# Optimization experiments

Hardware: AMD Instinct MI355X
Metric: run time of the kernel (lower is better)

Reference implementation:

```python
import jax, jax.numpy as jnp
import numpy as np
from jax.scipy.special import logsumexp

# Model config: alphabet='ACGTZY', collapse='ACGTCA' -> 4 canonical bases, 2 mods
NBASE = 4
NTRANS = 2 * NBASE * (NBASE + 1)          # 40 flip-flop transition states
CAN_NMODS = np.array([1, 1, 0, 0])        # mods per canonical base (A:Y, C:Z)
SIZE = NTRANS + 1 + int(CAN_NMODS.sum())  # 43 linear outputs
LARGE_LOG_VAL = np.float32(50000.0)
T, N, INSIZE = 2000, 128, 256


def _can_indices():
    """Per-canonical-base index groups into the mod block of the linear output."""
    idx, cur = [], 0
    for nm in CAN_NMODS:
        idx.append(np.concatenate([[0], np.arange(cur + 1, cur + 1 + nm)]))
        cur += nm
    return idx

CAN_INDICES = _can_indices()


def setup_inputs() -> dict:
    key = jax.random.key(0)
    k1, k2, k3 = jax.random.split(key, 3)
    x = jax.random.normal(k1, (T, N, INSIZE), dtype=jnp.float32)
    W = jax.random.normal(k2, (SIZE, INSIZE), dtype=jnp.float32) / np.float32(INSIZE ** 0.5)
    b = jax.random.normal(k3, (SIZE,), dtype=jnp.float32) * 0.1
    return {"x": x, "W": W, "b": b}


def global_norm_flipflop(scores):
    """Log-partition of the flip-flop CRF via a sequential log-space scan.

    scores: (T, N, 2*nbase*(nbase+1)).
    """
    Tn, Nn, _ = scores.shape
    # initial state: flip states uniform, flop states ~ -inf
    fwd0 = jnp.concatenate(
        [jnp.zeros((Nn, NBASE), scores.dtype),
         jnp.full((Nn, NBASE), -LARGE_LOG_VAL, scores.dtype)], axis=1)
    logZ0 = logsumexp(fwd0, axis=1, keepdims=True)
    fwd0 = fwd0 - logZ0

    def step(carry, scores_t):
        fwd, logZ = carry
        # (N, nbase+1, 2*nbase): dest-state x source-state transition scores
        curr = fwd[:, None, :] + scores_t.reshape(Nn, NBASE + 1, 2 * NBASE)
        base1 = logsumexp(curr[:, :NBASE], axis=2)                    # to-flip states
        base2 = jnp.logaddexp(curr[:, NBASE, :NBASE],
                              curr[:, NBASE, NBASE:])                 # to-flop (stay)
        new = jnp.concatenate([base1, base2], axis=1)                 # (N, 2*nbase)
        fac = logsumexp(new, axis=1, keepdims=True)
        return (new - fac, logZ + fac), None

    (_, logZ), _ = jax.lax.scan(step, (fwd0, logZ0), scores)
    return scores - logZ / np.float32(Tn)


def reference(x, W, b):
    # Linear projection: (T, N, insize) -> (T, N, size)
    y = jnp.einsum('tnf,cf->tnc', x, W) + b
    # Globally-normalized flip-flop transition scores
    trans = global_norm_flipflop(y[:, :, :NTRANS])
    # Per-canonical-base categorical (can + its mods) log-softmax scores
    mods = [jax.nn.log_softmax(y[:, :, NTRANS + idx], axis=2) for idx in CAN_INDICES]
    return jnp.concatenate([trans] + mods, axis=2)
```

## Files before the change

kernel.cpp:

```cpp
#include <hip/hip_runtime.h>

#define T_DIM 2000
#define N_DIM 128
#define IN_DIM 256
#define OUT_C 46
#define NROWS (T_DIM * N_DIM)
#define NCHUNK 250
#define CLEN 8
#define NSUPER 25
#define SLEN 10

typedef short bf16x8 __attribute__((ext_vector_type(8)));
typedef float f32x4 __attribute__((ext_vector_type(4)));

union F8U { bf16x8 v; uint32_t u[4]; };

__device__ __forceinline__ uint32_t cvtpk(float lo, float hi) {
  uint32_t r;
  asm("v_cvt_pk_bf16_f32 %0, %1, %2" : "=v"(r) : "v"(lo), "v"(hi));
  return r;
}

__device__ __forceinline__ float bf2f(unsigned short u) {
  uint32_t w = (uint32_t)u << 16;
  return __builtin_bit_cast(float, w);
}

#define LDSK 264

__global__ __launch_bounds__(256, 4) void k1_gemm(const float* __restrict__ x,
                                                  const float* __restrict__ W,
                                                  const float* __restrict__ b,
                                                  unsigned short* __restrict__ wsYT,
                                                  float* __restrict__ wsMod) {
  __shared__ unsigned short Wl[43 * LDSK];
  const int tid  = threadIdx.x;
  const int lane = tid & 63;
  const int wv   = tid >> 6;
  const int ln   = lane & 15;
  const int lh   = lane >> 4;

  {
    uint32_t* Wd = reinterpret_cast<uint32_t*>(Wl);
#pragma unroll
    for (int it = 0; it < 22; ++it) {
      int e = tid + it * 256;
      if (e < 43 * 128) {
        int n = e >> 7, kp = e & 127;
        float2 w = *reinterpret_cast<const float2*>(W + (size_t)n * IN_DIM + 2 * kp);
        Wd[n * (LDSK / 2) + kp] = cvtpk(w.x, w.y);
      }
    }
  }
  float bias[3];
#pragma unroll
  for (int nt = 0; nt < 3; ++nt) {
    int n = nt * 16 + ln;
    bias[nt] = b[n > 42 ? 42 : n];
  }
  __syncthreads();

  const int rowbase = blockIdx.x * 256 + wv * 64;
  const float* xbase = x + (size_t)(rowbase + ln) * IN_DIM + lh * 8;

  float4 bufA[8], bufB[8];
  f32x4 zero = {0.f, 0.f, 0.f, 0.f};
  f32x4 acc[3] = {zero, zero, zero};

#define LOADH(BUF, T, HF) do {                                               \
    const float* _p = xbase + (size_t)(T) * (16 * IN_DIM) + (HF) * 128;      \
    _Pragma("unroll")                                                        \
    for (int _s = 0; _s < 4; ++_s) {                                         \
      BUF[_s]     = *reinterpret_cast<const float4*>(_p + _s * 32);          \
      BUF[_s + 4] = *reinterpret_cast<const float4*>(_p + _s * 32 + 4);      \
    }                                                                        \
  } while (0)

#define COMPH(BUF, HF) do {                                                  \
    _Pragma("unroll")                                                        \
    for (int _s2 = 0; _s2 < 4; ++_s2) {                                      \
      F8U _af;                                                               \
      _af.u[0] = cvtpk(BUF[_s2].x, BUF[_s2].y);                              \
      _af.u[1] = cvtpk(BUF[_s2].z, BUF[_s2].w);                              \
      _af.u[2] = cvtpk(BUF[_s2 + 4].x, BUF[_s2 + 4].y);                      \
      _af.u[3] = cvtpk(BUF[_s2 + 4].z, BUF[_s2 + 4].w);                      \
      const int _s = (HF) * 4 + _s2;                                         \
      _Pragma("unroll")                                                      \
      for (int _nt = 0; _nt < 3; ++_nt) {                                    \
        const bf16x8 _bf = *reinterpret_cast<const bf16x8*>(                 \
            &Wl[(_nt * 16 + ln) * LDSK + _s * 32 + lh * 8]);                 \
        acc[_nt] = __builtin_amdgcn_mfma_f32_16x16x32_bf16(_af.v, _bf,       \
                                                           acc[_nt], 0, 0, 0);\
      }                                                                      \
    }                                                                        \
  } while (0)

  LOADH(bufA, 0, 0);
  LOADH(bufB, 0, 1);
#pragma unroll 1
  for (int t = 0; t < 4; ++t) {
    COMPH(bufA, 0);
    if (t < 3) LOADH(bufA, t + 1, 0);
    COMPH(bufB, 1);
    if (t < 3) LOADH(bufB, t + 1, 1);
    const int R0 = rowbase + t * 16;
    const int tt = R0 >> 7;
    const int n0 = (R0 & 127) + lh * 4;
#pragma unroll
    for (int nt = 0; nt < 3; ++nt) {
      const int c = nt * 16 + ln;
      if (nt < 2 || ln < 8) {
        uint32_t d0 = cvtpk(acc[nt][0] + bias[nt], acc[nt][1] + bias[nt]);
        uint32_t d1 = cvtpk(acc[nt][2] + bias[nt], acc[nt][3] + bias[nt]);
        uint2 v; v.x = d0; v.y = d1;
        *reinterpret_cast<uint2*>(wsYT + ((size_t)tt * 40 + c) * 128 + n0) = v;
      } else if (ln < 11) {
        float4 v;
        v.x = acc[2][0] + bias[2]; v.y = acc[2][1] + bias[2];
        v.z = acc[2][2] + bias[2]; v.w = acc[2][3] + bias[2];
        *reinterpret_cast<float4*>(
            wsMod + ((size_t)tt * 3 + (ln - 8)) * 128 + n0) = v;
      }
      acc[nt] = zero;
    }
  }
#undef LOADH
#undef COMPH
}

__global__ __launch_bounds__(256, 1) void k2a_chunk(const unsigned short* __restrict__ wsYT,
                                                    float* __restrict__ wsM,
                                                    float* __restrict__ wsScale) {
  const int g  = blockIdx.x * 256 + threadIdx.x;
  const int c  = g >> 7;
  const int n  = g & 127;
  const int t0 = c * CLEN;

  float M[8][8];
  float lsc = 0.f;
  float bufA[40], bufB[40];

#define LOADROW(BUF, TROW) do {                                              \
    const unsigned short* _yr = wsYT + (size_t)(TROW) * (40 * 128) + n;      \
    _Pragma("unroll")                                                        \
    for (int _q = 0; _q < 40; ++_q) BUF[_q] = bf2f(_yr[_q * 128]);           \
  } while (0)

#define INITM(BUF) do {                                                      \
    float _e[40];                                                            \
    _Pragma("unroll")                                                        \
    for (int _q = 0; _q < 40; ++_q) _e[_q] = __expf(BUF[_q]);                \
    _Pragma("unroll")                                                        \
    for (int _i = 0; _i < 4; ++_i)                                           \
      _Pragma("unroll")                                                      \
      for (int _j = 0; _j < 8; ++_j) M[_i][_j] = _e[8*_i+_j];                \
    _Pragma("unroll")                                                        \
    for (int _d = 0; _d < 4; ++_d) {                                         \
      _Pragma("unroll")                                                      \
      for (int _j = 0; _j < 8; ++_j) M[4+_d][_j] = 0.f;                      \
      M[4+_d][_d]   = _e[32+_d];                                             \
      M[4+_d][4+_d] = _e[36+_d];                                             \
    }                                                                        \
  } while (0)

#define STEPM(BUF) do {                                                      \
    float _e[40];                                                            \
    _Pragma("unroll")                                                        \
    for (int _q = 0; _q < 40; ++_q) _e[_q] = __expf(BUF[_q]);                \
    float _nm[8][8];                                                         \
    _Pragma("unroll")                                                        \
    for (int _j = 0; _j < 8; ++_j) {                                         \
      _Pragma("unroll")                                                      \
      for (int _i = 0; _i < 4; ++_i) {                                       \
        float _a = _e[8*_i+0]*M[0][_j] + _e[8*_i+1]*M[1][_j];                \
        float _b = _e[8*_i+2]*M[2][_j] + _e[8*_i+3]*M[3][_j];                \
        float _c = _e[8*_i+4]*M[4][_j] + _e[8*_i+5]*M[5][_j];                \
        float _d = _e[8*_i+6]*M[6][_j] + _e[8*_i+7]*M[7][_j];                \
        _nm[_i][_j] = (_a + _b) + (_c + _d);                                 \
      }                                                                      \
      _Pragma("unroll")                                                      \
      for (int _d2 = 0; _d2 < 4; ++_d2)                                      \
        _nm[4+_d2][_j] = _e[32+_d2]*M[_d2][_j] + _e[36+_d2]*M[4+_d2][_j];    \
    }                                                                        \
    _Pragma("unroll")                                                        \
    for (int _i = 0; _i < 8; ++_i)                                           \
      _Pragma("unroll")                                                      \
      for (int _j = 0; _j < 8; ++_j) M[_i][_j] = _nm[_i][_j];                \
  } while (0)

#define RENORM do {                                                          \
    float _S = 0.f;                                                          \
    _Pragma("unroll")                                                        \
    for (int _i = 0; _i < 8; ++_i)                                           \
      _Pragma("unroll")                                                      \
      for (int _j = 0; _j < 8; ++_j) _S += M[_i][_j];                        \
    lsc += __logf(_S);                                                       \
    const float _inv = 1.0f / _S;                                            \
    _Pragma("unroll")                                                        \
    for (int _i = 0; _i < 8; ++_i)                                           \
      _Pragma("unroll")                                                      \
      for (int _j = 0; _j < 8; ++_j) M[_i][_j] *= _inv;                      \
  } while (0)

  LOADROW(bufA, t0);
  LOADROW(bufB, t0 + 1);
  INITM(bufA);
  LOADROW(bufA, t0 + 2);
  STEPM(bufB);
  LOADROW(bufB, t0 + 3);
  STEPM(bufA);
  LOADROW(bufA, t0 + 4);
  STEPM(bufB);
  RENORM;
  LOADROW(bufB, t0 + 5);
  STEPM(bufA);
  LOADROW(bufA, t0 + 6);
  STEPM(bufB);
  LOADROW(bufB, t0 + 7);
  STEPM(bufA);
  STEPM(bufB);
  RENORM;

#undef LOADROW
#undef INITM
#undef STEPM
#undef RENORM

  float* dst = wsM + (size_t)(c * N_DIM + n) * 64;
#pragma unroll
  for (int q = 0; q < 16; ++q) {
    float4 v;
    v.x = M[q >> 1][(q & 1) * 4 + 0];
    v.y = M[q >> 1][(q & 1) * 4 + 1];
    v.z = M[q >> 1][(q & 1) * 4 + 2];
    v.w = M[q >> 1][(q & 1) * 4 + 3];
    reinterpret_cast<float4*>(dst)[q] = v;
  }
  wsScale[c * N_DIM + n] = lsc;
}

__global__ __launch_bounds__(128, 1) void k2c_super(const float* __restrict__ wsM,
                                                    const float* __restrict__ wsScale,
                                                    float* __restrict__ wsM2,
                                                    float* __restrict__ wsScale2) {
  const int sI = blockIdx.x;
  const int n  = threadIdx.x;
  const int c0 = sI * SLEN;

  float A[8][8], B0[8][8], B1[8][8];
  float lsc = 0.f;
#pragma unroll
  for (int u = 0; u < SLEN; ++u) lsc += wsScale[(c0 + u) * N_DIM + n];

#define LOADM(DST, CIDX) do {                                                \
    const float4* _p = reinterpret_cast<const float4*>(                      \
        wsM + (size_t)((CIDX) * N_DIM + n) * 64);                            \
    _Pragma("unroll")                                                        \
    for (int _q = 0; _q < 16; ++_q) {                                        \
      float4 _v = _p[_q];                                                    \
      DST[_q >> 1][(_q & 1) * 4 + 0] = _v.x;                                 \
      DST[_q >> 1][(_q & 1) * 4 + 1] = _v.y;                                 \
      DST[_q >> 1][(_q & 1) * 4 + 2] = _v.z;                                 \
      DST[_q >> 1][(_q & 1) * 4 + 3] = _v.w;                                 \
    }                                                                        \
  } while (0)

#define FOLD(BB) do {                                                        \
    float C[8][8];                                                           \
    _Pragma("unroll")                                                        \
    for (int _i = 0; _i < 8; ++_i)                                           \
      _Pragma("unroll")                                                      \
      for (int _j = 0; _j < 8; ++_j) {                                       \
        float _a = BB[_i][0]*A[0][_j] + BB[_i][1]*A[1][_j];                  \
        float _b = BB[_i][2]*A[2][_j] + BB[_i][3]*A[3][_j];                  \
        float _c = BB[_i][4]*A[4][_j] + BB[_i][5]*A[5][_j];                  \
        float _d = BB[_i][6]*A[6][_j] + BB[_i][7]*A[7][_j];                  \
        C[_i][_j] = (_a + _b) + (_c + _d);                                   \
      }                                                                      \
    float _S = 0.f;                                                          \
    _Pragma("unroll")                                                        \
    for (int _i = 0; _i < 8; ++_i)                                           \
      _Pragma("unroll")                                                      \
      for (int _j = 0; _j < 8; ++_j) _S += C[_i][_j];                        \
    lsc += __logf(_S);                                                       \
    const float _inv = 1.0f / _S;                                            \
    _Pragma("unroll")                                                        \
    for (int _i = 0; _i < 8; ++_i)                                           \
      _Pragma("unroll")                                                      \
      for (int _j = 0; _j < 8; ++_j) A[_i][_j] = C[_i][_j] * _inv;           \
  } while (0)

  LOADM(A, c0);
  LOADM(B0, c0 + 1);
  LOADM(B1, c0 + 2);
  FOLD(B0); LOADM(B0, c0 + 3);
  FOLD(B1); LOADM(B1, c0 + 4);
  FOLD(B0); LOADM(B0, c0 + 5);
  FOLD(B1); LOADM(B1, c0 + 6);
  FOLD(B0); LOADM(B0, c0 + 7);
  FOLD(B1); LOADM(B1, c0 + 8);
  FOLD(B0); LOADM(B0, c0 + 9);
  FOLD(B1);
  FOLD(B0);
#undef LOADM
#undef FOLD

  float* dst = wsM2 + (size_t)(sI * N_DIM + n) * 64;
#pragma unroll
  for (int q = 0; q < 16; ++q) {
    float4 v;
    v.x = A[q >> 1][(q & 1) * 4 + 0];
    v.y = A[q >> 1][(q & 1) * 4 + 1];
    v.z = A[q >> 1][(q & 1) * 4 + 2];
    v.w = A[q >> 1][(q & 1) * 4 + 3];
    reinterpret_cast<float4*>(dst)[q] = v;
  }
  wsScale2[sI * N_DIM + n] = lsc;
}

__global__ __launch_bounds__(128, 1) void k2b_fold(const float* __restrict__ wsM2,
                                                   const float* __restrict__ wsScale2,
                                                   float* __restrict__ wsLZ) {
  const int tid = threadIdx.x;
  const int n = blockIdx.x * 16 + (tid >> 3);
  const int i = tid & 7;
  const int gbase = (tid & 63) & ~7;

  float4 r0[NSUPER], r1[NSUPER];
  float sc[NSUPER];
#pragma unroll
  for (int s = 0; s < NSUPER; ++s) {
    const float* Mp = wsM2 + ((size_t)(s * N_DIM + n) * 64 + i * 8);
    r0[s] = *reinterpret_cast<const float4*>(Mp);
    r1[s] = *reinterpret_cast<const float4*>(Mp + 4);
    sc[s] = wsScale2[s * N_DIM + n];
  }

  float p[8] = {1.f, 1.f, 1.f, 1.f, 0.f, 0.f, 0.f, 0.f};
  float lz = 0.f;
#pragma unroll
  for (int s = 0; s < NSUPER; ++s) {
    float np = r0[s].x * p[0] + r0[s].y * p[1] + r0[s].z * p[2] + r0[s].w * p[3]
             + r1[s].x * p[4] + r1[s].y * p[5] + r1[s].z * p[6] + r1[s].w * p[7];
#pragma unroll
    for (int j = 0; j < 8; ++j) p[j] = __shfl(np, gbase + j, 64);
    float S = ((p[0] + p[1]) + (p[2] + p[3])) + ((p[4] + p[5]) + (p[6] + p[7]));
    lz += __logf(S) + sc[s];
    const float inv = 1.0f / S;
#pragma unroll
    for (int j = 0; j < 8; ++j) p[j] *= inv;
  }
  if (i == 0) wsLZ[n] = lz * (1.0f / (float)T_DIM);
}

__global__ __launch_bounds__(256, 3) void k3_out(const unsigned short* __restrict__ wsYT,
                                                 const float* __restrict__ wsMod,
                                                 const float* __restrict__ wsLZ,
                                                 float* __restrict__ out) {
  __shared__ float L[256 * 47];
  const int tid = threadIdx.x;
  const int fr  = blockIdx.x * 256 + tid;
  const int t   = fr >> 7;
  const int n   = fr & 127;
  const float sub = wsLZ[n];

  const unsigned short* yr = wsYT + (size_t)t * (40 * 128) + n;
  float* lrow = &L[tid * 47];
#pragma unroll
  for (int c = 0; c < 40; ++c) lrow[c] = bf2f(yr[c * 128]) - sub;

  const float* mp = wsMod + (size_t)t * (3 * 128) + n;
  const float y40 = mp[0], y41 = mp[128], y42 = mp[256];
  const float m01 = fmaxf(y40, y41);
  const float l01 = m01 + log1pf(__expf(fminf(y40, y41) - m01));
  const float m02 = fmaxf(y40, y42);
  const float l02 = m02 + log1pf(__expf(fminf(y40, y42) - m02));
  lrow[40] = y40 - l01;
  lrow[41] = y41 - l01;
  lrow[42] = y40 - l02;
  lrow[43] = y42 - l02;
  lrow[44] = 0.f;
  lrow[45] = 0.f;
  __syncthreads();

  const size_t base = (size_t)blockIdx.x * (256 * 46);
#pragma unroll
  for (int j = 0; j < 46; ++j) {
    const int e = j * 256 + tid;
    const int r = e / 46;
    const int c = e - r * 46;
    out[base + e] = L[r * 47 + c];
  }
}

extern "C" void kernel_launch(void* const* d_in, const int* in_sizes, int n_in,
                              void* d_out, int out_size, void* d_ws, size_t ws_size,
                              hipStream_t stream) {
  (void)in_sizes; (void)n_in; (void)out_size; (void)ws_size;
  const float* x = (const float*)d_in[0];
  const float* W = (const float*)d_in[1];
  const float* b = (const float*)d_in[2];
  float* out = (float*)d_out;

  char* wsb = (char*)d_ws;
  unsigned short* wsYT = (unsigned short*)wsb;
  float* wsMod   = (float*)(wsb + (size_t)T_DIM * 40 * 128 * 2);
  float* wsM     = wsMod + (size_t)T_DIM * 3 * N_DIM;
  float* wsScale = wsM + (size_t)NCHUNK * N_DIM * 64;
  float* wsM2    = wsScale + NCHUNK * N_DIM;
  float* wsScale2= wsM2 + (size_t)NSUPER * N_DIM * 64;
  float* wsLZ    = wsScale2 + NSUPER * N_DIM;

  hipLaunchKernelGGL(k1_gemm,   dim3(NROWS / 256), dim3(256), 0, stream,
                     x, W, b, wsYT, wsMod);
  hipLaunchKernelGGL(k2a_chunk, dim3(NCHUNK * N_DIM / 256), dim3(256), 0, stream,
                     wsYT, wsM, wsScale);
  hipLaunchKernelGGL(k2c_super, dim3(NSUPER), dim3(128), 0, stream,
                     wsM, wsScale, wsM2, wsScale2);
  hipLaunchKernelGGL(k2b_fold,  dim3(8), dim3(128), 0, stream,
                     wsM2, wsScale2, wsLZ);
  hipLaunchKernelGGL(k3_out,    dim3(NROWS / 256), dim3(256), 0, stream,
                     wsYT, wsMod, wsLZ, out);
}
```

Before: 116.1 us.

## Retune block sizes, add nontemporal x loads, vectorize output kernel reads

The GEMM kernel moves to 512-thread blocks and loads x through nontemporal loads so the streamed input does not pollute cache. The chunk kernel drops to 64-thread blocks to spread the small grid across more CUs. The output kernel now uses 128 threads that each handle two batch columns, with 32-bit paired bf16 loads and float2 mod loads to cut load instruction count. The tradeoff is fewer threads per block for the store transpose and different occupancy behavior.

```diff
diff --git a/kernel.cpp b/kernel.cpp
--- a/kernel.cpp
+++ b/kernel.cpp
@@ -28,7 +28,7 @@
 
 #define LDSK 264
 
-__global__ __launch_bounds__(256, 4) void k1_gemm(const float* __restrict__ x,
+__global__ __launch_bounds__(512, 2) void k1_gemm(const float* __restrict__ x,
                                                   const float* __restrict__ W,
                                                   const float* __restrict__ b,
                                                   unsigned short* __restrict__ wsYT,
@@ -43,8 +43,8 @@
   {
     uint32_t* Wd = reinterpret_cast<uint32_t*>(Wl);
 #pragma unroll
-    for (int it = 0; it < 22; ++it) {
-      int e = tid + it * 256;
+    for (int it = 0; it < 11; ++it) {
+      int e = tid + it * 512;
       if (e < 43 * 128) {
         int n = e >> 7, kp = e & 127;
         float2 w = *reinterpret_cast<const float2*>(W + (size_t)n * IN_DIM + 2 * kp);
@@ -60,10 +60,10 @@
   }
   __syncthreads();
 
-  const int rowbase = blockIdx.x * 256 + wv * 64;
+  const int rowbase = blockIdx.x * 512 + wv * 64;
   const float* xbase = x + (size_t)(rowbase + ln) * IN_DIM + lh * 8;
 
-  float4 bufA[8], bufB[8];
+  f32x4 bufA[8], bufB[8];
   f32x4 zero = {0.f, 0.f, 0.f, 0.f};
   f32x4 acc[3] = {zero, zero, zero};
 
@@ -71,8 +71,10 @@
     const float* _p = xbase + (size_t)(T) * (16 * IN_DIM) + (HF) * 128;      \
     _Pragma("unroll")                                                        \
     for (int _s = 0; _s < 4; ++_s) {                                         \
-      BUF[_s]     = *reinterpret_cast<const float4*>(_p + _s * 32);          \
-      BUF[_s + 4] = *reinterpret_cast<const float4*>(_p + _s * 32 + 4);      \
+      BUF[_s]     = __builtin_nontemporal_load(                              \
+          reinterpret_cast<const f32x4*>(_p + _s * 32));                     \
+      BUF[_s + 4] = __builtin_nontemporal_load(                              \
+          reinterpret_cast<const f32x4*>(_p + _s * 32 + 4));                 \
     }                                                                        \
   } while (0)
 
@@ -128,10 +130,10 @@
 #undef COMPH
 }
 
-__global__ __launch_bounds__(256, 1) void k2a_chunk(const unsigned short* __restrict__ wsYT,
-                                                    float* __restrict__ wsM,
-                                                    float* __restrict__ wsScale) {
-  const int g  = blockIdx.x * 256 + threadIdx.x;
+__global__ __launch_bounds__(64, 1) void k2a_chunk(const unsigned short* __restrict__ wsYT,
+                                                   float* __restrict__ wsM,
+                                                   float* __restrict__ wsScale) {
+  const int g  = blockIdx.x * 64 + threadIdx.x;
   const int c  = g >> 7;
   const int n  = g & 127;
   const int t0 = c * CLEN;
@@ -353,40 +355,51 @@
   if (i == 0) wsLZ[n] = lz * (1.0f / (float)T_DIM);
 }
 
-__global__ __launch_bounds__(256, 3) void k3_out(const unsigned short* __restrict__ wsYT,
+__global__ __launch_bounds__(128, 3) void k3_out(const unsigned short* __restrict__ wsYT,
                                                  const float* __restrict__ wsMod,
                                                  const float* __restrict__ wsLZ,
                                                  float* __restrict__ out) {
   __shared__ float L[256 * 47];
   const int tid = threadIdx.x;
-  const int fr  = blockIdx.x * 256 + tid;
-  const int t   = fr >> 7;
-  const int n   = fr & 127;
-  const float sub = wsLZ[n];
-
-  const unsigned short* yr = wsYT + (size_t)t * (40 * 128) + n;
-  float* lrow = &L[tid * 47];
-#pragma unroll
-  for (int c = 0; c < 40; ++c) lrow[c] = bf2f(yr[c * 128]) - sub;
-
-  const float* mp = wsMod + (size_t)t * (3 * 128) + n;
-  const float y40 = mp[0], y41 = mp[128], y42 = mp[256];
-  const float m01 = fmaxf(y40, y41);
-  const float l01 = m01 + log1pf(__expf(fminf(y40, y41) - m01));
-  const float m02 = fmaxf(y40, y42);
-  const float l02 = m02 + log1pf(__expf(fminf(y40, y42) - m02));
-  lrow[40] = y40 - l01;
-  lrow[41] = y41 - l01;
-  lrow[42] = y40 - l02;
-  lrow[43] = y42 - l02;
-  lrow[44] = 0.f;
-  lrow[45] = 0.f;
+  const int tp  = tid >> 6;
+  const int np  = tid & 63;
+  const int t   = blockIdx.x * 2 + tp;
+  const int n0  = np * 2;
+
+  const float2 sub2 = *reinterpret_cast<const float2*>(wsLZ + n0);
+  const unsigned short* yr = wsYT + (size_t)t * (40 * 128) + n0;
+  float* r0 = &L[(tp * 128 + n0) * 47];
+  float* r1 = r0 + 47;
+#pragma unroll
+  for (int c = 0; c < 40; ++c) {
+    uint32_t v = *reinterpret_cast<const uint32_t*>(yr + c * 128);
+    r0[c] = bf2f((unsigned short)(v & 0xFFFF)) - sub2.x;
+    r1[c] = bf2f((unsigned short)(v >> 16)) - sub2.y;
+  }
+
+  const float* mp = wsMod + (size_t)t * (3 * 128) + n0;
+  const float2 y40 = *reinterpret_cast<const float2*>(mp);
+  const float2 y41 = *reinterpret_cast<const float2*>(mp + 128);
+  const float2 y42 = *reinterpret_cast<const float2*>(mp + 256);
+
+#define MODROW(R, A, B, C)  do {                                             \
+    const float m01 = fmaxf(A, B);                                           \
+    const float l01 = m01 + log1pf(__expf(fminf(A, B) - m01));               \
+    const float m02 = fmaxf(A, C);                                           \
+    const float l02 = m02 + log1pf(__expf(fminf(A, C) - m02));               \
+    R[40] = A - l01; R[41] = B - l01;                                        \
+    R[42] = A - l02; R[43] = C - l02;                                        \
+    R[44] = 0.f;     R[45] = 0.f;                                            \
+  } while (0)
+  MODROW(r0, y40.x, y41.x, y42.x);
+  MODROW(r1, y40.y, y41.y, y42.y);
+#undef MODROW
   __syncthreads();
 
   const size_t base = (size_t)blockIdx.x * (256 * 46);
 #pragma unroll
-  for (int j = 0; j < 46; ++j) {
-    const int e = j * 256 + tid;
+  for (int j = 0; j < 92; ++j) {
+    const int e = j * 128 + tid;
     const int r = e / 46;
     const int c = e - r * 46;
     out[base + e] = L[r * 47 + c];
@@ -411,14 +424,14 @@
   float* wsScale2= wsM2 + (size_t)NSUPER * N_DIM * 64;
   float* wsLZ    = wsScale2 + NSUPER * N_DIM;
 
-  hipLaunchKernelGGL(k1_gemm,   dim3(NROWS / 256), dim3(256), 0, stream,
+  hipLaunchKernelGGL(k1_gemm,   dim3(NROWS / 512), dim3(512), 0, stream,
                      x, W, b, wsYT, wsMod);
-  hipLaunchKernelGGL(k2a_chunk, dim3(NCHUNK * N_DIM / 256), dim3(256), 0, stream,
+  hipLaunchKernelGGL(k2a_chunk, dim3(NCHUNK * N_DIM / 64), dim3(64), 0, stream,
                      wsYT, wsM, wsScale);
   hipLaunchKernelGGL(k2c_super, dim3(NSUPER), dim3(128), 0, stream,
                      wsM, wsScale, wsM2, wsScale2);
   hipLaunchKernelGGL(k2b_fold,  dim3(8), dim3(128), 0, stream,
                      wsM2, wsScale2, wsLZ);
-  hipLaunchKernelGGL(k3_out,    dim3(NROWS / 256), dim3(256), 0, stream,
+  hipLaunchKernelGGL(k3_out,    dim3(NROWS / 256), dim3(128), 0, stream,
                      wsYT, wsMod, wsLZ, out);
 }
```

Result: slower. 123.8 us (+6.7%).
